# Kernel optimization log

Measured on AMD Instinct MI355X. Metric: run time of the kernel, lower is better.

Reference implementation:

```python
import jax, jax.numpy as jnp
import numpy as np


def _onedirectional_dist(a, b):
    # a: [B, Na], b: [B, Nb] -> sum over Na of nearest-neighbor squared distance
    d2 = (a[:, :, None] - b[:, None, :]) ** 2          # [B, Na, Nb]
    d2 = jnp.where(jnp.isfinite(d2), d2, jnp.inf)      # mask non-finite -> inf
    nn_d2 = jnp.min(d2, axis=2)                        # [B, Na]
    nn_d2 = jnp.where(jnp.isfinite(nn_d2), nn_d2, 0.0) # all-inf rows -> 0
    return nn_d2.sum(axis=1)                           # [B]


def setup_inputs() -> dict:
    key = jax.random.key(0)
    k1, k2 = jax.random.split(key)
    # B=1 (the torch broadcast target/target_max only works for B==1 w/o mask)
    target = jax.random.uniform(k1, (1, 1, 480, 640), jnp.float32, 0.1, 10.0)
    bin_centers = jax.random.uniform(k2, (1, 256), jnp.float32, 0.1, 10.0)
    return {"target": target, "bin_centers": bin_centers}


def reference(target, bin_centers):
    # scale_invariant=True, mask=None path
    target_max = jnp.max(target, axis=(2, 3))       # [B, 1]
    bin_centers_max = jnp.max(bin_centers, axis=1)  # [B]
    target_n = target / target_max                  # per-image normalization (B==1)
    bin_centers_n = bin_centers / bin_centers_max
    target_depths = target_n.reshape(target_n.shape[0], -1)  # [B, H*W]
    bidir = _onedirectional_dist(bin_centers_n, target_depths) \
          + _onedirectional_dist(target_depths, bin_centers_n)
    return bidir.mean()
```

## Files before the change

kernel.cpp:

```cpp
#include <hip/hip_runtime.h>
#include <math.h>

#define THREADS 256
#define BPB 8
#define PCH 16

__device__ __forceinline__ float wredMax(float v) {
  #pragma unroll
  for (int o = 32; o > 0; o >>= 1) v = fmaxf(v, __shfl_down(v, o, 64));
  return v;
}
__device__ __forceinline__ float wredMin(float v) {
  #pragma unroll
  for (int o = 32; o > 0; o >>= 1) v = fminf(v, __shfl_down(v, o, 64));
  return v;
}
__device__ __forceinline__ float wredSum(float v) {
  #pragma unroll
  for (int o = 32; o > 0; o >>= 1) v += __shfl_down(v, o, 64);
  return v;
}


__global__ __launch_bounds__(THREADS) void k_tmax(const float4* __restrict__ t4, int n4,
                                                  const float* __restrict__ t, int n,
                                                  unsigned int* __restrict__ wsu) {
  __shared__ float sm[4];
  float v = 0.0f;
  int idx = blockIdx.x * THREADS + threadIdx.x;
  int stride = gridDim.x * THREADS;
  for (int i = idx; i < n4; i += stride) {
    float4 a = t4[i];
    v = fmaxf(v, fmaxf(fmaxf(a.x, a.y), fmaxf(a.z, a.w)));
  }
  for (int i = n4 * 4 + idx; i < n; i += stride) v = fmaxf(v, t[i]);
  v = wredMax(v);
  int lane = threadIdx.x & 63, wid = threadIdx.x >> 6;
  if (lane == 0) sm[wid] = v;
  __syncthreads();
  if (threadIdx.x == 0) {
    float m = fmaxf(fmaxf(sm[0], sm[1]), fmaxf(sm[2], sm[3]));
    atomicMax(wsu, __float_as_uint(m));
  }
}

__global__ __launch_bounds__(THREADS) void k_main(const float4* __restrict__ t4, int n4,
                                                  const float* __restrict__ t, int n,
                                                  const float* __restrict__ bins, int nb,
                                                  const unsigned int* __restrict__ wsu,
                                                  double* __restrict__ wsum,
                                                  unsigned int* __restrict__ binmin,
                                                  int t1b) {
  __shared__ float sred[4];
  __shared__ float sm[4 * BPB];
  __shared__ float bsh[1024];

  const int lane = threadIdx.x & 63, wid = threadIdx.x >> 6;

  float bv = 0.0f;
  for (int i = threadIdx.x; i < nb; i += THREADS) bv = fmaxf(bv, bins[i]);
  bv = wredMax(bv);
  if (lane == 0) sred[wid] = bv;
  __syncthreads();
  const float ib = 1.0f / fmaxf(fmaxf(sred[0], sred[1]), fmaxf(sred[2], sred[3]));
  const float it = 1.0f / __uint_as_float(wsu[0]);
  __syncthreads();

  if ((int)blockIdx.x < t1b) {
    const int g = blockIdx.x / PCH;
    const int c = blockIdx.x % PCH;
    const int base = g * BPB;
    float bn[BPB], mn[BPB];
    #pragma unroll
    for (int k = 0; k < BPB; k++) {
      int bi = base + k;
      bn[k] = (bi < nb) ? bins[bi] * ib : 3e30f;
      mn[k] = 1e30f;
    }
    const int chunk = (n4 + PCH - 1) / PCH;
    const int lo = c * chunk;
    const int hi = (lo + chunk < n4) ? lo + chunk : n4;
    for (int i = lo + threadIdx.x; i < hi; i += THREADS) {
      float4 a = t4[i];
      float tn[4] = {a.x * it, a.y * it, a.z * it, a.w * it};
      #pragma unroll
      for (int k = 0; k < BPB; k++) {
        #pragma unroll
        for (int cc = 0; cc < 4; cc++) {
          float d = bn[k] - tn[cc];
          mn[k] = fminf(mn[k], d * d);
        }
      }
    }
    if (c == 0) {
      for (int i = n4 * 4 + threadIdx.x; i < n; i += THREADS) {
        float tn = t[i] * it;
        #pragma unroll
        for (int k = 0; k < BPB; k++) {
          float d = bn[k] - tn;
          mn[k] = fminf(mn[k], d * d);
        }
      }
    }
    #pragma unroll
    for (int k = 0; k < BPB; k++) {
      float m = wredMin(mn[k]);
      if (lane == 0) sm[wid * BPB + k] = m;
    }
    __syncthreads();
    if (threadIdx.x < BPB) {
      int k = threadIdx.x;
      if (base + k < nb) {
        float m = fminf(fminf(sm[k], sm[BPB + k]), fminf(sm[2 * BPB + k], sm[3 * BPB + k]));
        atomicMin(&binmin[base + k], __float_as_uint(m));
      }
    }
  } else {
    for (int i = threadIdx.x; i < nb && i < 1024; i += THREADS) bsh[i] = bins[i] * ib;
    __syncthreads();
    const int b2 = blockIdx.x - t1b;
    const int stride = (gridDim.x - t1b) * THREADS;
    float lsum = 0.0f;
    for (int i = b2 * THREADS + threadIdx.x; i < n4; i += stride) {
      float4 a = t4[i];
      float t0 = a.x * it, t1 = a.y * it, t2 = a.z * it, t3 = a.w * it;
      float m0 = 1e30f, m1 = 1e30f, m2 = 1e30f, m3 = 1e30f;
      #pragma unroll 4
      for (int j = 0; j < nb; j++) {
        float b = bsh[j];
        float d0 = t0 - b, d1 = t1 - b, d2 = t2 - b, d3 = t3 - b;
        m0 = fminf(m0, d0 * d0);
        m1 = fminf(m1, d1 * d1);
        m2 = fminf(m2, d2 * d2);
        m3 = fminf(m3, d3 * d3);
      }
      lsum += (m0 + m1) + (m2 + m3);
    }
    for (int i = n4 * 4 + b2 * THREADS + threadIdx.x; i < n; i += stride) {
      float tn = t[i] * it;
      float m = 1e30f;
      for (int j = 0; j < nb; j++) {
        float d = tn - bsh[j];
        m = fminf(m, d * d);
      }
      lsum += m;
    }
    float s = wredSum(lsum);
    if (lane == 0) sred[wid] = s;
    __syncthreads();
    if (threadIdx.x == 0)
      atomicAdd(wsum, (double)((sred[0] + sred[1]) + (sred[2] + sred[3])));
  }
}

__global__ __launch_bounds__(THREADS) void k_fin(const unsigned int* __restrict__ binmin, int nb,
                                                 const double* __restrict__ wsum,
                                                 float* __restrict__ out) {
  __shared__ float sm[4];
  float s = 0.0f;
  for (int i = threadIdx.x; i < nb; i += THREADS) {
    float m = __uint_as_float(binmin[i]);
    s += (m < 1e30f) ? m : 0.0f;
  }
  s = wredSum(s);
  int lane = threadIdx.x & 63, wid = threadIdx.x >> 6;
  if (lane == 0) sm[wid] = s;
  __syncthreads();
  if (threadIdx.x == 0)
    out[0] = (float)(wsum[0] + (double)((sm[0] + sm[1]) + (sm[2] + sm[3])));
}

extern "C" void kernel_launch(void* const* d_in, const int* in_sizes, int n_in,
                              void* d_out, int out_size, void* d_ws, size_t ws_size,
                              hipStream_t stream) {
  const float* target = (const float*)d_in[0];
  const float* bins = (const float*)d_in[1];
  const int n = in_sizes[0];
  const int nb = in_sizes[1];
  float* out = (float*)d_out;

  unsigned int* wsu = (unsigned int*)d_ws;
  double* wsum = (double*)((char*)d_ws + 8);
  unsigned int* binmin = (unsigned int*)((char*)d_ws + 16);

  const int n4 = n / 4;
  const float4* t4 = (const float4*)target;

  hipMemsetAsync(d_ws, 0, 16, stream);
  hipMemsetAsync((char*)d_ws + 16, 0x7F, (size_t)4 * nb, stream);

  int gmax = (n4 + THREADS - 1) / THREADS;
  if (gmax > 512) gmax = 512;
  if (gmax < 1) gmax = 1;
  k_tmax<<<gmax, THREADS, 0, stream>>>(t4, n4, target, n, wsu);

  const int t1b = ((nb + BPB - 1) / BPB) * PCH;
  const int n2b = 300;
  k_main<<<t1b + n2b, THREADS, 0, stream>>>(t4, n4, target, n, bins, nb, wsu, wsum, binmin, t1b);

  k_fin<<<1, THREADS, 0, stream>>>(binmin, nb, wsum, out);
}
```

Before: 78.32 us.

## Fuse both NN directions per block with last-block reduction and expanded-square distances

Both distance directions now run in every block of a single main kernel instead of separate block roles. The closing reduction is done by the last-arriving block via an atomic ticket, which removes the finalize kernel and both memsets. The max kernel writes per-wave partial maxima that each block reduces, replacing a float atomicMax. Distances use the expanded form b^2 - 2tb + t^2 with FMAs so the inner loops do fewer ops, at some risk of cancellation error when t and b are close.

```diff
diff --git a/kernel.cpp b/kernel.cpp
--- a/kernel.cpp
+++ b/kernel.cpp
@@ -4,28 +4,34 @@
 #define THREADS 256
 #define BPB 8
 #define PCH 16
-
-__device__ __forceinline__ float wredMax(float v) {
-  #pragma unroll
-  for (int o = 32; o > 0; o >>= 1) v = fmaxf(v, __shfl_down(v, o, 64));
-  return v;
-}
-__device__ __forceinline__ float wredMin(float v) {
-  #pragma unroll
-  for (int o = 32; o > 0; o >>= 1) v = fminf(v, __shfl_down(v, o, 64));
-  return v;
-}
-__device__ __forceinline__ float wredSum(float v) {
-  #pragma unroll
-  for (int o = 32; o > 0; o >>= 1) v += __shfl_down(v, o, 64);
-  return v;
-}
-
+#define TMAXB 128
+
+
+__device__ __forceinline__ float wmaxAll(float v) {
+  #pragma unroll
+  for (int o = 32; o > 0; o >>= 1) v = fmaxf(v, __shfl_xor(v, o, 64));
+  return v;
+}
+__device__ __forceinline__ float wminAll(float v) {
+  #pragma unroll
+  for (int o = 32; o > 0; o >>= 1) v = fminf(v, __shfl_xor(v, o, 64));
+  return v;
+}
+__device__ __forceinline__ float wsumAll(float v) {
+  #pragma unroll
+  for (int o = 32; o > 0; o >>= 1) v += __shfl_xor(v, o, 64);
+  return v;
+}
+__device__ __forceinline__ double wsumAllD(double v) {
+  #pragma unroll
+  for (int o = 32; o > 0; o >>= 1) v += __shfl_xor(v, o, 64);
+  return v;
+}
 
 __global__ __launch_bounds__(THREADS) void k_tmax(const float4* __restrict__ t4, int n4,
                                                   const float* __restrict__ t, int n,
-                                                  unsigned int* __restrict__ wsu) {
-  __shared__ float sm[4];
+                                                  float* __restrict__ pmax,
+                                                  unsigned int* __restrict__ counter) {
   float v = 0.0f;
   int idx = blockIdx.x * THREADS + threadIdx.x;
   int stride = gridDim.x * THREADS;
@@ -34,140 +40,141 @@
     v = fmaxf(v, fmaxf(fmaxf(a.x, a.y), fmaxf(a.z, a.w)));
   }
   for (int i = n4 * 4 + idx; i < n; i += stride) v = fmaxf(v, t[i]);
-  v = wredMax(v);
-  int lane = threadIdx.x & 63, wid = threadIdx.x >> 6;
-  if (lane == 0) sm[wid] = v;
-  __syncthreads();
-  if (threadIdx.x == 0) {
-    float m = fmaxf(fmaxf(sm[0], sm[1]), fmaxf(sm[2], sm[3]));
-    atomicMax(wsu, __float_as_uint(m));
-  }
+  v = wmaxAll(v);
+  int lane = threadIdx.x & 63, w = threadIdx.x >> 6;
+  if (lane == 0) pmax[blockIdx.x * 4 + w] = v;
+  if (idx == 0) *counter = 0u;
 }
 
 __global__ __launch_bounds__(THREADS) void k_main(const float4* __restrict__ t4, int n4,
                                                   const float* __restrict__ t, int n,
                                                   const float* __restrict__ bins, int nb,
-                                                  const unsigned int* __restrict__ wsu,
-                                                  double* __restrict__ wsum,
-                                                  unsigned int* __restrict__ binmin,
-                                                  int t1b) {
-  __shared__ float sred[4];
-  __shared__ float sm[4 * BPB];
-  __shared__ float bsh[1024];
-
-  const int lane = threadIdx.x & 63, wid = threadIdx.x >> 6;
-
+                                                  const float* __restrict__ pmax,
+                                                  float* __restrict__ psum,
+                                                  float* __restrict__ pmin,
+                                                  unsigned int* __restrict__ counter,
+                                                  float* __restrict__ out, int G) {
+  __shared__ float sb[1024], hb[1024];
+  __shared__ float sm1[4 * BPB];
+  __shared__ float ss[4];
+  __shared__ double ds[4];
+  __shared__ unsigned int ticket;
+
+  const int tid = threadIdx.x;
+  const int lane = tid & 63, w = tid >> 6;
+  const int bid = blockIdx.x;
+
+  float v = 0.0f;
+  for (int i = lane; i < TMAXB * 4; i += 64) v = fmaxf(v, pmax[i]);
+  const float it = 1.0f / wmaxAll(v);
   float bv = 0.0f;
-  for (int i = threadIdx.x; i < nb; i += THREADS) bv = fmaxf(bv, bins[i]);
-  bv = wredMax(bv);
-  if (lane == 0) sred[wid] = bv;
+  for (int i = lane; i < nb; i += 64) bv = fmaxf(bv, bins[i]);
+  const float ib = 1.0f / wmaxAll(bv);
+
+  for (int i = tid; i < nb && i < 1024; i += THREADS) {
+    float b = bins[i] * ib;
+    sb[i] = b * b;
+    hb[i] = -(b + b);
+  }
   __syncthreads();
-  const float ib = 1.0f / fmaxf(fmaxf(sred[0], sred[1]), fmaxf(sred[2], sred[3]));
-  const float it = 1.0f / __uint_as_float(wsu[0]);
-  __syncthreads();
-
-  if ((int)blockIdx.x < t1b) {
-    const int g = blockIdx.x / PCH;
-    const int c = blockIdx.x % PCH;
-    const int base = g * BPB;
-    float bn[BPB], mn[BPB];
-    #pragma unroll
-    for (int k = 0; k < BPB; k++) {
-      int bi = base + k;
-      bn[k] = (bi < nb) ? bins[bi] * ib : 3e30f;
-      mn[k] = 1e30f;
-    }
+
+  float lsum = 0.0f;
+  {
+    int idx = bid * THREADS + tid;
+    if (idx < n4) {
+      float4 a = t4[idx];
+      float t0 = a.x * it, t1 = a.y * it, t2 = a.z * it, t3 = a.w * it;
+      float m0 = 1e30f, m1 = 1e30f, m2 = 1e30f, m3 = 1e30f;
+      #pragma unroll 8
+      for (int j = 0; j < nb; j++) {
+        float s = sb[j], h = hb[j];
+        m0 = fminf(m0, fmaf(h, t0, s));
+        m1 = fminf(m1, fmaf(h, t1, s));
+        m2 = fminf(m2, fmaf(h, t2, s));
+        m3 = fminf(m3, fmaf(h, t3, s));
+      }
+      lsum = (fmaf(t0, t0, m0) + fmaf(t1, t1, m1)) + (fmaf(t2, t2, m2) + fmaf(t3, t3, m3));
+    }
+    int ntail = n - n4 * 4;
+    if (bid == 0 && tid < ntail) {
+      float tv = t[n4 * 4 + tid] * it;
+      float m = 1e30f;
+      for (int j = 0; j < nb; j++) m = fminf(m, fmaf(hb[j], tv, sb[j]));
+      lsum += fmaf(tv, tv, m);
+    }
+  }
+
+  const int g = bid / PCH, c = bid % PCH;
+  const int base = g * BPB;
+  float bn[BPB], mn[BPB];
+  #pragma unroll
+  for (int k = 0; k < BPB; k++) {
+    int bi = base + k;
+    bn[k] = (bi < nb) ? bins[bi] * ib : 3e30f;
+    mn[k] = 1e30f;
+  }
+  {
     const int chunk = (n4 + PCH - 1) / PCH;
     const int lo = c * chunk;
     const int hi = (lo + chunk < n4) ? lo + chunk : n4;
-    for (int i = lo + threadIdx.x; i < hi; i += THREADS) {
+    for (int i = lo + tid; i < hi; i += THREADS) {
       float4 a = t4[i];
-      float tn[4] = {a.x * it, a.y * it, a.z * it, a.w * it};
+      float t0 = a.x * it, t1 = a.y * it, t2 = a.z * it, t3 = a.w * it;
+      float s0 = t0 * t0, s1 = t1 * t1, s2 = t2 * t2, s3 = t3 * t3;
+      float h0 = -(t0 + t0), h1 = -(t1 + t1), h2 = -(t2 + t2), h3 = -(t3 + t3);
       #pragma unroll
       for (int k = 0; k < BPB; k++) {
-        #pragma unroll
-        for (int cc = 0; cc < 4; cc++) {
-          float d = bn[k] - tn[cc];
-          mn[k] = fminf(mn[k], d * d);
-        }
+        float b = bn[k];
+        mn[k] = fminf(mn[k], fmaf(h0, b, s0));
+        mn[k] = fminf(mn[k], fmaf(h1, b, s1));
+        mn[k] = fminf(mn[k], fmaf(h2, b, s2));
+        mn[k] = fminf(mn[k], fmaf(h3, b, s3));
       }
     }
-    if (c == 0) {
-      for (int i = n4 * 4 + threadIdx.x; i < n; i += THREADS) {
-        float tn = t[i] * it;
-        #pragma unroll
-        for (int k = 0; k < BPB; k++) {
-          float d = bn[k] - tn;
-          mn[k] = fminf(mn[k], d * d);
-        }
-      }
-    }
-    #pragma unroll
-    for (int k = 0; k < BPB; k++) {
-      float m = wredMin(mn[k]);
-      if (lane == 0) sm[wid * BPB + k] = m;
-    }
+    int ntail = n - n4 * 4;
+    if (c == 0 && tid < ntail) {
+      float tv = t[n4 * 4 + tid] * it;
+      float s = tv * tv, h = -(tv + tv);
+      #pragma unroll
+      for (int k = 0; k < BPB; k++) mn[k] = fminf(mn[k], fmaf(h, bn[k], s));
+    }
+  }
+
+  #pragma unroll
+  for (int k = 0; k < BPB; k++) {
+    float m = wminAll(mn[k]);
+    if (lane == 0) sm1[w * BPB + k] = m;
+  }
+  float s = wsumAll(lsum);
+  if (lane == 0) ss[w] = s;
+  __syncthreads();
+  if (tid == 0) psum[bid] = (ss[0] + ss[1]) + (ss[2] + ss[3]);
+  if (tid < BPB && base + tid < nb) {
+    float m = fminf(fminf(sm1[tid], sm1[BPB + tid]),
+                    fminf(sm1[2 * BPB + tid], sm1[3 * BPB + tid]));
+    pmin[(base + tid) * PCH + c] = m;
+  }
+
+  __threadfence();
+  if (tid == 0) ticket = atomicAdd(counter, 1u);
+  __syncthreads();
+  if (ticket == (unsigned int)(G - 1)) {
+    __threadfence();
+    double tsum = 0.0;
+    for (int b = tid; b < nb; b += THREADS) {
+      float m = 1e30f;
+      #pragma unroll
+      for (int cc = 0; cc < PCH; cc++) m = fminf(m, pmin[b * PCH + cc]);
+      float bnv = bins[b] * ib;
+      float val = fmaf(bnv, bnv, m);
+      tsum += (m < 1e30f) ? (double)val : 0.0;
+    }
+    for (int i = tid; i < G; i += THREADS) tsum += (double)psum[i];
+    tsum = wsumAllD(tsum);
+    if (lane == 0) ds[w] = tsum;
     __syncthreads();
-    if (threadIdx.x < BPB) {
-      int k = threadIdx.x;
-      if (base + k < nb) {
-        float m = fminf(fminf(sm[k], sm[BPB + k]), fminf(sm[2 * BPB + k], sm[3 * BPB + k]));
-        atomicMin(&binmin[base + k], __float_as_uint(m));
-      }
-    }
-  } else {
-    for (int i = threadIdx.x; i < nb && i < 1024; i += THREADS) bsh[i] = bins[i] * ib;
-    __syncthreads();
-    const int b2 = blockIdx.x - t1b;
-    const int stride = (gridDim.x - t1b) * THREADS;
-    float lsum = 0.0f;
-    for (int i = b2 * THREADS + threadIdx.x; i < n4; i += stride) {
-      float4 a = t4[i];
-      float t0 = a.x * it, t1 = a.y * it, t2 = a.z * it, t3 = a.w * it;
-      float m0 = 1e30f, m1 = 1e30f, m2 = 1e30f, m3 = 1e30f;
-      #pragma unroll 4
-      for (int j = 0; j < nb; j++) {
-        float b = bsh[j];
-        float d0 = t0 - b, d1 = t1 - b, d2 = t2 - b, d3 = t3 - b;
-        m0 = fminf(m0, d0 * d0);
-        m1 = fminf(m1, d1 * d1);
-        m2 = fminf(m2, d2 * d2);
-        m3 = fminf(m3, d3 * d3);
-      }
-      lsum += (m0 + m1) + (m2 + m3);
-    }
-    for (int i = n4 * 4 + b2 * THREADS + threadIdx.x; i < n; i += stride) {
-      float tn = t[i] * it;
-      float m = 1e30f;
-      for (int j = 0; j < nb; j++) {
-        float d = tn - bsh[j];
-        m = fminf(m, d * d);
-      }
-      lsum += m;
-    }
-    float s = wredSum(lsum);
-    if (lane == 0) sred[wid] = s;
-    __syncthreads();
-    if (threadIdx.x == 0)
-      atomicAdd(wsum, (double)((sred[0] + sred[1]) + (sred[2] + sred[3])));
-  }
-}
-
-__global__ __launch_bounds__(THREADS) void k_fin(const unsigned int* __restrict__ binmin, int nb,
-                                                 const double* __restrict__ wsum,
-                                                 float* __restrict__ out) {
-  __shared__ float sm[4];
-  float s = 0.0f;
-  for (int i = threadIdx.x; i < nb; i += THREADS) {
-    float m = __uint_as_float(binmin[i]);
-    s += (m < 1e30f) ? m : 0.0f;
-  }
-  s = wredSum(s);
-  int lane = threadIdx.x & 63, wid = threadIdx.x >> 6;
-  if (lane == 0) sm[wid] = s;
-  __syncthreads();
-  if (threadIdx.x == 0)
-    out[0] = (float)(wsum[0] + (double)((sm[0] + sm[1]) + (sm[2] + sm[3])));
+    if (tid == 0) out[0] = (float)(((ds[0] + ds[1]) + (ds[2] + ds[3])));
+  }
 }
 
 extern "C" void kernel_launch(void* const* d_in, const int* in_sizes, int n_in,
@@ -179,24 +186,17 @@
   const int nb = in_sizes[1];
   float* out = (float*)d_out;
 
-  unsigned int* wsu = (unsigned int*)d_ws;
-  double* wsum = (double*)((char*)d_ws + 8);
-  unsigned int* binmin = (unsigned int*)((char*)d_ws + 16);
+  unsigned int* counter = (unsigned int*)d_ws;
+  float* pmax = (float*)((char*)d_ws + 256);
+  float* psum = (float*)((char*)d_ws + 4096);
+  float* pmin = (float*)((char*)d_ws + 8192);
 
   const int n4 = n / 4;
   const float4* t4 = (const float4*)target;
 
-  hipMemsetAsync(d_ws, 0, 16, stream);
-  hipMemsetAsync((char*)d_ws + 16, 0x7F, (size_t)4 * nb, stream);
-
-  int gmax = (n4 + THREADS - 1) / THREADS;
-  if (gmax > 512) gmax = 512;
-  if (gmax < 1) gmax = 1;
-  k_tmax<<<gmax, THREADS, 0, stream>>>(t4, n4, target, n, wsu);
-
-  const int t1b = ((nb + BPB - 1) / BPB) * PCH;
-  const int n2b = 300;
-  k_main<<<t1b + n2b, THREADS, 0, stream>>>(t4, n4, target, n, bins, nb, wsu, wsum, binmin, t1b);
-
-  k_fin<<<1, THREADS, 0, stream>>>(binmin, nb, wsum, out);
-}
+  k_tmax<<<TMAXB, THREADS, 0, stream>>>(t4, n4, target, n, pmax, counter);
+
+  const int G = ((nb + BPB - 1) / BPB) * PCH;
+  k_main<<<G, THREADS, 0, stream>>>(t4, n4, target, n, bins, nb, pmax, psum, pmin,
+                                    counter, out, G);
+}
```

Result: slower. 106.4 us (+35.9%).
